# Performance work log

Hardware: AMD Instinct MI355X
Metric: run time of the kernel (lower is better)

## Reference

```python
import jax, jax.numpy as jnp
import numpy as np

B, S, H, D = 8, 2048, 8, 64  # x: [batch, seq, heads, emb_size]; emb_size is per-head dim here


def setup_inputs() -> dict:
    key = jax.random.key(0)
    ks = jax.random.split(key, 9)
    s = 1.0 / np.sqrt(D)
    return {
        "x": jax.random.normal(ks[0], (B, S, H, D), dtype=jnp.float32),
        "Wq": jax.random.uniform(ks[1], (D, D), jnp.float32, -s, s),
        "bq": jax.random.uniform(ks[2], (D,), jnp.float32, -s, s),
        "Wk": jax.random.uniform(ks[3], (D, D), jnp.float32, -s, s),
        "bk": jax.random.uniform(ks[4], (D,), jnp.float32, -s, s),
        "Wv": jax.random.uniform(ks[5], (D, D), jnp.float32, -s, s),
        "bv": jax.random.uniform(ks[6], (D,), jnp.float32, -s, s),
        "Wo": jax.random.uniform(ks[7], (D, D), jnp.float32, -s, s),
        "bo": jax.random.uniform(ks[8], (D,), jnp.float32, -s, s),
    }


def reference(x, Wq, bq, Wk, bk, Wv, bv, Wo, bo):
    # Linear projections on last dim, then permute(0,2,1,3): [b,s,h,d] -> [b,h,s,d]
    q = jnp.einsum('bshd,ed->bhse', x, Wq) + bq
    k = jnp.einsum('bshd,ed->bhse', x, Wk) + bk
    v = jnp.einsum('bshd,ed->bhse', x, Wv) + bv
    energy = jnp.einsum('bhqd,bhkd->bhqk', q, k)  # full O(S^2) score matrix
    scaling = jnp.asarray(D, jnp.float32) ** 0.5  # emb_size ** (1/2), applied post-matmul
    att = jax.nn.softmax(energy / scaling, axis=-1)
    out = jnp.einsum('bhqk,bhkd->bhqd', att, v)
    out = jnp.transpose(out, (0, 2, 1, 3))  # back to [b,s,h,d]
    return jnp.einsum('bshd,ed->bshe', out, Wo) + bo
```

## Files before the change

kernel.cpp:

```cpp
#include <hip/hip_runtime.h>
#include <hip/hip_bf16.h>

#define Bc 8
#define Sc 2048
#define Hc 8
#define Dc 64

#define SCALE_LOG2E 0.18033688011112042f

typedef __bf16 bf16x8 __attribute__((ext_vector_type(8)));
typedef __bf16 bf16x4 __attribute__((ext_vector_type(4)));
typedef float f32x4 __attribute__((ext_vector_type(4)));
typedef float f32x16 __attribute__((ext_vector_type(16)));
typedef int i32x4 __attribute__((ext_vector_type(4)));

__device__ __forceinline__ f32x4 mfma16(bf16x8 a, bf16x8 b, f32x4 c) {
  return __builtin_amdgcn_mfma_f32_16x16x32_bf16(a, b, c, 0, 0, 0);
}
__device__ __forceinline__ f32x16 mfma32(bf16x8 a, bf16x8 b, f32x16 c) {
  return __builtin_amdgcn_mfma_f32_32x32x16_bf16(a, b, c, 0, 0, 0);
}

__device__ __forceinline__ bf16x8 cvt8(const float* __restrict__ p) {
  bf16x8 r;
#pragma unroll
  for (int i = 0; i < 8; ++i) r[i] = (__bf16)p[i];
  return r;
}

__device__ __forceinline__ f32x4 zero4() {
  f32x4 z = {0.f, 0.f, 0.f, 0.f};
  return z;
}
__device__ __forceinline__ f32x16 zero16() {
  f32x16 z;
#pragma unroll
  for (int i = 0; i < 16; ++i) z[i] = 0.f;
  return z;
}

__device__ __forceinline__ unsigned pkbf16(float lo, float hi) {
  unsigned r;
  asm("v_cvt_pk_bf16_f32 %0, %1, %2" : "=v"(r) : "v"(lo), "v"(hi));
  return r;
}

typedef __attribute__((address_space(1))) void as1_void;
typedef __attribute__((address_space(3))) void as3_void;

__device__ __forceinline__ void lds_load16(const void* gsrc, void* ldst) {
  __builtin_amdgcn_global_load_lds((as1_void*)(void*)gsrc, (as3_void*)ldst, 16, 0, 0);
}

__global__ __launch_bounds__(256) void qkv_kernel(
    const float* __restrict__ x,
    const float* __restrict__ Wq, const float* __restrict__ bq,
    const float* __restrict__ Wk, const float* __restrict__ bk,
    const float* __restrict__ Wv, const float* __restrict__ bv,
    __bf16* __restrict__ Qb, __bf16* __restrict__ Kb, __bf16* __restrict__ Vt)
{
  const int tid = threadIdx.x;
  const int wid = tid >> 6;
  const int lane = tid & 63;
  const int lr = lane & 15;
  const int lg = lane >> 4;

  const int bid = blockIdx.x;
  const int st = bid & 7;
  const int h  = (bid >> 3) & 7;
  const int b  = bid >> 6;
  const int bh = b * Hc + h;

  bf16x8 wqf[4][2], wkf[4][2], wvf[4][2];
#pragma unroll
  for (int cb = 0; cb < 4; ++cb)
#pragma unroll
    for (int dc = 0; dc < 2; ++dc) {
      const int off = (cb * 16 + lr) * Dc + dc * 32 + lg * 8;
      wqf[cb][dc] = cvt8(Wq + off);
      wkf[cb][dc] = cvt8(Wk + off);
      wvf[cb][dc] = cvt8(Wv + off);
    }
  f32x4 bqv[4], bkv[4], bvv[4];
#pragma unroll
  for (int cb = 0; cb < 4; ++cb) {
    bqv[cb] = *(const f32x4*)(bq + cb * 16 + lg * 4);
    bkv[cb] = *(const f32x4*)(bk + cb * 16 + lg * 4);
    bvv[cb] = *(const f32x4*)(bv + cb * 16 + lg * 4);
  }

#pragma unroll 1
  for (int it = 0; it < 4; ++it) {
    const int s0 = st * 256 + it * 64 + wid * 16;
    bf16x8 xf[2];
#pragma unroll
    for (int dc = 0; dc < 2; ++dc)
      xf[dc] = cvt8(x + ((size_t)(b * Sc + s0 + lr) * Hc + h) * Dc + dc * 32 + lg * 8);

    const size_t row = (size_t)bh * Sc + s0 + lr;
#pragma unroll
    for (int cb = 0; cb < 4; ++cb) {
      f32x4 aq = zero4(), ak = zero4();
      aq = mfma16(wqf[cb][0], xf[0], aq);
      aq = mfma16(wqf[cb][1], xf[1], aq);
      ak = mfma16(wkf[cb][0], xf[0], ak);
      ak = mfma16(wkf[cb][1], xf[1], ak);
      bf16x4 qpk, kpk;
#pragma unroll
      for (int rr = 0; rr < 4; ++rr) {
        qpk[rr] = (__bf16)((aq[rr] + bqv[cb][rr]) * SCALE_LOG2E);
        kpk[rr] = (__bf16)(ak[rr] + bkv[cb][rr]);
      }
      *(bf16x4*)(Qb + row * Dc + cb * 16 + lg * 4) = qpk;
      *(bf16x4*)(Kb + row * Dc + cb * 16 + lg * 4) = kpk;
    }
#pragma unroll
    for (int eb = 0; eb < 4; ++eb) {
      f32x4 av = zero4();
      av = mfma16(wvf[eb][0], xf[0], av);
      av = mfma16(wvf[eb][1], xf[1], av);
#pragma unroll
      for (int rr = 0; rr < 4; ++rr) {
        const int e = eb * 16 + lg * 4 + rr;
        Vt[((size_t)bh * Dc + e) * Sc + s0 + lr] = (__bf16)(av[rr] + bvv[eb][rr]);
      }
    }
  }
}

__global__ __launch_bounds__(256) void attn_kernel(
    const __bf16* __restrict__ Qb, const __bf16* __restrict__ Kb,
    const __bf16* __restrict__ Vt, const float* __restrict__ Wo,
    const float* __restrict__ bo, float* __restrict__ out)
{
  __shared__ __align__(16) __bf16 kls[2][64 * 64];
  __shared__ __align__(16) __bf16 vls[2][64 * 64];

  const int tid = threadIdx.x;
  const int wid = tid >> 6;
  const int lane = tid & 63;
  const int l31 = lane & 31;
  const int hi = lane >> 5;

  const int bid = blockIdx.x;
  const int bh = bid & 63;
  const int qb = bid >> 6;
  const int b = bh >> 3, h = bh & 7;
  const int q0 = qb * 128 + wid * 32;

  const __bf16* Kbase = Kb + (size_t)bh * Sc * Dc;
  const __bf16* Vbase = Vt + (size_t)bh * Dc * Sc;

  bf16x8 qf[4];
#pragma unroll
  for (int slot = 0; slot < 4; ++slot)
    qf[slot] = *(const bf16x8*)(Qb + ((size_t)bh * Sc + q0 + l31) * Dc +
                                slot * 16 + hi * 8);

  f32x16 ot[2];
  ot[0] = zero16();
  ot[1] = zero16();
  float lsum = 0.f;

#pragma unroll
  for (int i = 0; i < 2; ++i) {
    const int s = i * 256 + tid, r = s >> 3, c = s & 7;
    lds_load16(Kbase + (size_t)r * Dc + ((c ^ (r & 7)) * 8),
               &kls[0][(i * 256 + wid * 64) * 8]);
  }
#pragma unroll
  for (int i = 0; i < 2; ++i) {
    const int s = i * 256 + tid, d = s >> 3, c = s & 7;
    lds_load16(Vbase + (size_t)d * Sc + ((c ^ (d & 7)) * 8),
               &vls[0][(i * 256 + wid * 64) * 8]);
  }

#pragma unroll 1
  for (int kt = 0; kt < Sc / 64; ++kt) {
    const int cur = kt & 1;
    const int nk0 = ((kt + 1) & 31) * 64;
    __builtin_amdgcn_sched_barrier(0);
#pragma unroll
    for (int i = 0; i < 2; ++i) {
      const int s = i * 256 + tid, r = s >> 3, c = s & 7;
      lds_load16(Kbase + (size_t)(nk0 + r) * Dc + ((c ^ (r & 7)) * 8),
                 &kls[cur ^ 1][(i * 256 + wid * 64) * 8]);
    }
#pragma unroll
    for (int i = 0; i < 2; ++i) {
      const int s = i * 256 + tid, d = s >> 3, c = s & 7;
      lds_load16(Vbase + (size_t)d * Sc + nk0 + ((c ^ (d & 7)) * 8),
                 &vls[cur ^ 1][(i * 256 + wid * 64) * 8]);
    }
    asm volatile("s_waitcnt vmcnt(4)" ::: "memory");
    __builtin_amdgcn_sched_barrier(0);
    __builtin_amdgcn_s_barrier();
    __builtin_amdgcn_sched_barrier(0);

    f32x16 e[2];
    e[0] = zero16();
    e[1] = zero16();
    __builtin_amdgcn_s_setprio(1);
#pragma unroll
    for (int kg = 0; kg < 2; ++kg) {
      const int r = kg * 32 + l31;
#pragma unroll
      for (int slot = 0; slot < 4; ++slot) {
        bf16x8 kf = *(const bf16x8*)(
            &kls[cur][r * 64 + (((slot * 2 + hi) ^ (r & 7)) * 8)]);
        e[kg] = mfma32(kf, qf[slot], e[kg]);
      }
    }
    __builtin_amdgcn_s_setprio(0);

#pragma unroll
    for (int kg = 0; kg < 2; ++kg)
#pragma unroll
      for (int i = 0; i < 16; ++i) {
        const float p = __builtin_amdgcn_exp2f(e[kg][i]);
        e[kg][i] = p;
        lsum += p;
      }

    unsigned pw[4][4];
#pragma unroll
    for (int kg = 0; kg < 2; ++kg)
#pragma unroll
      for (int hf = 0; hf < 2; ++hf) {
        unsigned a0 = pkbf16(e[kg][8 * hf + 0], e[kg][8 * hf + 1]);
        unsigned a1 = pkbf16(e[kg][8 * hf + 2], e[kg][8 * hf + 3]);
        unsigned b0 = pkbf16(e[kg][8 * hf + 4], e[kg][8 * hf + 5]);
        unsigned b1 = pkbf16(e[kg][8 * hf + 6], e[kg][8 * hf + 7]);
        asm volatile("v_permlane32_swap_b32 %0, %1" : "+v"(a0), "+v"(b0));
        asm volatile("v_permlane32_swap_b32 %0, %1" : "+v"(a1), "+v"(b1));
        const int slot = 2 * kg + hf;
        pw[slot][0] = a0; pw[slot][1] = a1; pw[slot][2] = b0; pw[slot][3] = b1;
      }

    __builtin_amdgcn_s_setprio(1);
#pragma unroll
    for (int dg = 0; dg < 2; ++dg) {
      const int r = dg * 32 + l31;
#pragma unroll
      for (int slot = 0; slot < 4; ++slot) {
        bf16x8 vf = *(const bf16x8*)(
            &vls[cur][r * 64 + (((slot * 2 + hi) ^ (r & 7)) * 8)]);
        i32x4 w = {(int)pw[slot][0], (int)pw[slot][1],
                   (int)pw[slot][2], (int)pw[slot][3]};
        ot[dg] = mfma32(vf, __builtin_bit_cast(bf16x8, w), ot[dg]);
      }
    }
    __builtin_amdgcn_s_setprio(0);

    __builtin_amdgcn_s_barrier();
  }

  lsum += __shfl_xor(lsum, 32);
  const float linv = __builtin_amdgcn_rcpf(lsum);
#pragma unroll
  for (int dg = 0; dg < 2; ++dg)
#pragma unroll
    for (int i = 0; i < 16; ++i) ot[dg][i] *= linv;

  unsigned ow[4][4];
#pragma unroll
  for (int dg = 0; dg < 2; ++dg)
#pragma unroll
    for (int hf = 0; hf < 2; ++hf) {
      unsigned a0 = pkbf16(ot[dg][8 * hf + 0], ot[dg][8 * hf + 1]);
      unsigned a1 = pkbf16(ot[dg][8 * hf + 2], ot[dg][8 * hf + 3]);
      unsigned b0 = pkbf16(ot[dg][8 * hf + 4], ot[dg][8 * hf + 5]);
      unsigned b1 = pkbf16(ot[dg][8 * hf + 6], ot[dg][8 * hf + 7]);
      asm volatile("v_permlane32_swap_b32 %0, %1" : "+v"(a0), "+v"(b0));
      asm volatile("v_permlane32_swap_b32 %0, %1" : "+v"(a1), "+v"(b1));
      const int slot = 2 * dg + hf;
      ow[slot][0] = a0; ow[slot][1] = a1; ow[slot][2] = b0; ow[slot][3] = b1;
    }

  f32x16 oacc[2];
  oacc[0] = zero16();
  oacc[1] = zero16();
#pragma unroll
  for (int eg = 0; eg < 2; ++eg) {
#pragma unroll
    for (int slot = 0; slot < 4; ++slot) {
      bf16x8 wf = cvt8(Wo + (eg * 32 + l31) * Dc + slot * 16 + hi * 8);
      i32x4 w = {(int)ow[slot][0], (int)ow[slot][1],
                 (int)ow[slot][2], (int)ow[slot][3]};
      oacc[eg] = mfma32(wf, __builtin_bit_cast(bf16x8, w), oacc[eg]);
    }
  }

  const size_t srow = ((size_t)b * Sc + q0 + l31) * Hc + h;
#pragma unroll
  for (int eg = 0; eg < 2; ++eg)
#pragma unroll
    for (int c = 0; c < 4; ++c) {
      const f32x4 bo4 = *(const f32x4*)(bo + eg * 32 + c * 8 + hi * 4);
      f32x4 v;
#pragma unroll
      for (int j = 0; j < 4; ++j) v[j] = oacc[eg][4 * c + j] + bo4[j];
      *(f32x4*)(out + srow * Dc + eg * 32 + c * 8 + hi * 4) = v;
    }
}

extern "C" void kernel_launch(void* const* d_in, const int* in_sizes, int n_in,
                              void* d_out, int out_size, void* d_ws, size_t ws_size,
                              hipStream_t stream) {
  const float* x  = (const float*)d_in[0];
  const float* Wq = (const float*)d_in[1];
  const float* bq = (const float*)d_in[2];
  const float* Wk = (const float*)d_in[3];
  const float* bk = (const float*)d_in[4];
  const float* Wv = (const float*)d_in[5];
  const float* bv = (const float*)d_in[6];
  const float* Wo = (const float*)d_in[7];
  const float* bo = (const float*)d_in[8];
  float* outp = (float*)d_out;

  const size_t elems = (size_t)Bc * Hc * Sc * Dc;
  __bf16* Qw = (__bf16*)d_ws;
  __bf16* Kw = Qw + elems;
  __bf16* Vw = Kw + elems;

  qkv_kernel<<<dim3(Bc * Hc * 8), dim3(256), 0, stream>>>(
      x, Wq, bq, Wk, bk, Wv, bv, Qw, Kw, Vw);
  attn_kernel<<<dim3(Bc * Hc * (Sc / 128)), dim3(256), 0, stream>>>(
      Qw, Kw, Vw, Wo, bo, outp);
}
```

Baseline: 220.3 us.

## Triple-buffer K/V LDS tiles to drop trailing barrier; repartition QKV projection by output column

The attention kernel moves from double to triple buffering of the K and V shared-memory tiles. This removes the end-of-iteration barrier, so only one barrier per key tile remains. The cost is 16KB more LDS per block, which may reduce occupancy. The QKV projection kernel now gives each wave a 16-wide slice of output columns for all 64 rows instead of 16 rows across all columns. That cuts the weight registers each wave holds, but each wave now loads more x fragments.

```diff
diff --git a/kernel.cpp b/kernel.cpp
--- a/kernel.cpp
+++ b/kernel.cpp
@@ -70,59 +70,54 @@
   const int h  = (bid >> 3) & 7;
   const int b  = bid >> 6;
   const int bh = b * Hc + h;
-
-  bf16x8 wqf[4][2], wkf[4][2], wvf[4][2];
-#pragma unroll
-  for (int cb = 0; cb < 4; ++cb)
-#pragma unroll
-    for (int dc = 0; dc < 2; ++dc) {
-      const int off = (cb * 16 + lr) * Dc + dc * 32 + lg * 8;
-      wqf[cb][dc] = cvt8(Wq + off);
-      wkf[cb][dc] = cvt8(Wk + off);
-      wvf[cb][dc] = cvt8(Wv + off);
-    }
-  f32x4 bqv[4], bkv[4], bvv[4];
-#pragma unroll
-  for (int cb = 0; cb < 4; ++cb) {
-    bqv[cb] = *(const f32x4*)(bq + cb * 16 + lg * 4);
-    bkv[cb] = *(const f32x4*)(bk + cb * 16 + lg * 4);
-    bvv[cb] = *(const f32x4*)(bv + cb * 16 + lg * 4);
-  }
+  const int e0 = wid * 16;
+
+  bf16x8 wqf[2], wkf[2], wvf[2];
+#pragma unroll
+  for (int dc = 0; dc < 2; ++dc) {
+    const int off = (e0 + lr) * Dc + dc * 32 + lg * 8;
+    wqf[dc] = cvt8(Wq + off);
+    wkf[dc] = cvt8(Wk + off);
+    wvf[dc] = cvt8(Wv + off);
+  }
+  const f32x4 bqv = *(const f32x4*)(bq + e0 + lg * 4);
+  const f32x4 bkv = *(const f32x4*)(bk + e0 + lg * 4);
+  const f32x4 bvv = *(const f32x4*)(bv + e0 + lg * 4);
 
 #pragma unroll 1
   for (int it = 0; it < 4; ++it) {
-    const int s0 = st * 256 + it * 64 + wid * 16;
-    bf16x8 xf[2];
-#pragma unroll
-    for (int dc = 0; dc < 2; ++dc)
-      xf[dc] = cvt8(x + ((size_t)(b * Sc + s0 + lr) * Hc + h) * Dc + dc * 32 + lg * 8);
-
-    const size_t row = (size_t)bh * Sc + s0 + lr;
-#pragma unroll
-    for (int cb = 0; cb < 4; ++cb) {
-      f32x4 aq = zero4(), ak = zero4();
-      aq = mfma16(wqf[cb][0], xf[0], aq);
-      aq = mfma16(wqf[cb][1], xf[1], aq);
-      ak = mfma16(wkf[cb][0], xf[0], ak);
-      ak = mfma16(wkf[cb][1], xf[1], ak);
+    const int s0 = st * 256 + it * 64;
+    bf16x8 xf[4][2];
+#pragma unroll
+    for (int sc = 0; sc < 4; ++sc)
+#pragma unroll
+      for (int dc = 0; dc < 2; ++dc)
+        xf[sc][dc] = cvt8(x + ((size_t)(b * Sc + s0 + sc * 16 + lr) * Hc + h) * Dc +
+                          dc * 32 + lg * 8);
+
+#pragma unroll
+    for (int sc = 0; sc < 4; ++sc) {
+      const size_t row = (size_t)bh * Sc + s0 + sc * 16 + lr;
+      f32x4 aq = zero4(), ak = zero4(), av = zero4();
+      aq = mfma16(wqf[0], xf[sc][0], aq);
+      aq = mfma16(wqf[1], xf[sc][1], aq);
+      ak = mfma16(wkf[0], xf[sc][0], ak);
+      ak = mfma16(wkf[1], xf[sc][1], ak);
+      av = mfma16(wvf[0], xf[sc][0], av);
+      av = mfma16(wvf[1], xf[sc][1], av);
       bf16x4 qpk, kpk;
 #pragma unroll
       for (int rr = 0; rr < 4; ++rr) {
-        qpk[rr] = (__bf16)((aq[rr] + bqv[cb][rr]) * SCALE_LOG2E);
-        kpk[rr] = (__bf16)(ak[rr] + bkv[cb][rr]);
-      }
-      *(bf16x4*)(Qb + row * Dc + cb * 16 + lg * 4) = qpk;
-      *(bf16x4*)(Kb + row * Dc + cb * 16 + lg * 4) = kpk;
-    }
-#pragma unroll
-    for (int eb = 0; eb < 4; ++eb) {
-      f32x4 av = zero4();
-      av = mfma16(wvf[eb][0], xf[0], av);
-      av = mfma16(wvf[eb][1], xf[1], av);
+        qpk[rr] = (__bf16)((aq[rr] + bqv[rr]) * SCALE_LOG2E);
+        kpk[rr] = (__bf16)(ak[rr] + bkv[rr]);
+      }
+      *(bf16x4*)(Qb + row * Dc + e0 + lg * 4) = qpk;
+      *(bf16x4*)(Kb + row * Dc + e0 + lg * 4) = kpk;
 #pragma unroll
       for (int rr = 0; rr < 4; ++rr) {
-        const int e = eb * 16 + lg * 4 + rr;
-        Vt[((size_t)bh * Dc + e) * Sc + s0 + lr] = (__bf16)(av[rr] + bvv[eb][rr]);
+        const int e = e0 + lg * 4 + rr;
+        Vt[((size_t)bh * Dc + e) * Sc + s0 + sc * 16 + lr] =
+            (__bf16)(av[rr] + bvv[rr]);
       }
     }
   }
@@ -133,8 +128,8 @@
     const __bf16* __restrict__ Vt, const float* __restrict__ Wo,
     const float* __restrict__ bo, float* __restrict__ out)
 {
-  __shared__ __align__(16) __bf16 kls[2][64 * 64];
-  __shared__ __align__(16) __bf16 vls[2][64 * 64];
+  __shared__ __align__(16) __bf16 kls[3][64 * 64];
+  __shared__ __align__(16) __bf16 vls[3][64 * 64];
 
   const int tid = threadIdx.x;
   const int wid = tid >> 6;
@@ -175,22 +170,24 @@
                &vls[0][(i * 256 + wid * 64) * 8]);
   }
 
+  int cur = 0;
 #pragma unroll 1
   for (int kt = 0; kt < Sc / 64; ++kt) {
-    const int cur = kt & 1;
+    int stg = cur + 1;
+    if (stg == 3) stg = 0;
     const int nk0 = ((kt + 1) & 31) * 64;
     __builtin_amdgcn_sched_barrier(0);
 #pragma unroll
     for (int i = 0; i < 2; ++i) {
       const int s = i * 256 + tid, r = s >> 3, c = s & 7;
       lds_load16(Kbase + (size_t)(nk0 + r) * Dc + ((c ^ (r & 7)) * 8),
-                 &kls[cur ^ 1][(i * 256 + wid * 64) * 8]);
+                 &kls[stg][(i * 256 + wid * 64) * 8]);
     }
 #pragma unroll
     for (int i = 0; i < 2; ++i) {
       const int s = i * 256 + tid, d = s >> 3, c = s & 7;
       lds_load16(Vbase + (size_t)d * Sc + nk0 + ((c ^ (d & 7)) * 8),
-                 &vls[cur ^ 1][(i * 256 + wid * 64) * 8]);
+                 &vls[stg][(i * 256 + wid * 64) * 8]);
     }
     asm volatile("s_waitcnt vmcnt(4)" ::: "memory");
     __builtin_amdgcn_sched_barrier(0);
@@ -252,7 +249,7 @@
     }
     __builtin_amdgcn_s_setprio(0);
 
-    __builtin_amdgcn_s_barrier();
+    cur = stg;
   }
 
   lsum += __shfl_xor(lsum, 32);
```

Result: no change. 224.2 us (+1.8%).
